# Kernel tuning notes

Hardware: AMD Instinct MI355X
Metric: run time of the kernel (lower is better)

Reference implementation:

```python
import jax, jax.numpy as jnp
import numpy as np

B, S, D = 8, 2048, 1024
N = 256          # state_dim
H = 512          # selector_hidden
E = 8            # num_experts


def murmurhash3_finalizer(token_ids):
    # Torch code works in int64 but masks to 32 bits after each multiply and
    # values stay non-negative, so it is exactly uint32 wrapping arithmetic.
    x = token_ids.astype(jnp.uint32)
    x = x ^ (x >> 16)
    x = x * jnp.uint32(2246822507)
    x = x ^ (x >> 13)
    x = x * jnp.uint32(3266489909)
    x = x ^ (x >> 16)
    return x


def setup_inputs() -> dict:
    key = jax.random.key(0)
    ks = jax.random.split(key, 7)
    scale = 0.02
    return {
        "x": jax.random.normal(ks[0], (B, S, D), dtype=jnp.float32),
        "token_ids": jax.random.randint(ks[1], (B, S), 0, 50257, dtype=jnp.int32),
        "Win": jax.random.normal(ks[2], (E, N, D), dtype=jnp.float32) * scale,      # in_proj.weight per expert
        "Wsin": jax.random.normal(ks[3], (E, H, D), dtype=jnp.float32) * scale,     # selector_in.weight
        "Wsout": jax.random.normal(ks[4], (E, 4 * N, H), dtype=jnp.float32) * scale,  # selector_out.weight
        "Wout": jax.random.normal(ks[5], (E, D, N), dtype=jnp.float32) * scale,     # out_proj.weight
        "dparam": jnp.ones((E, N), dtype=jnp.float32),                              # per-expert d
    }


def _forward(x, Win, Wsin, Wsout, Wout, dparam, token_ids):
    b, s, d = x.shape
    e_num, n, _ = Win.shape
    routes = (murmurhash3_finalizer(token_ids) % jnp.uint32(e_num)).astype(jnp.int32)  # (B,S)

    # Per-token expert projections, selected by hash route (masked accumulation
    # over the small fixed expert count; honors per-token routing).
    u = jnp.zeros((b, s, n), x.dtype)
    a = jnp.zeros((b, s, n), x.dtype)
    bg = jnp.zeros((b, s, n), x.dtype)
    c = jnp.zeros((b, s, n), x.dtype)
    dg = jnp.zeros((b, s, n), x.dtype)
    for e in range(e_num):
        m = (routes == e)[..., None]
        u = jnp.where(m, jnp.einsum('bsd,nd->bsn', x, Win[e]), u)
        sh = jax.nn.silu(jnp.einsum('bsd,hd->bsh', x, Wsin[e]))
        sel = jnp.einsum('bsh,oh->bso', sh, Wsout[e])       # (B,S,4N)
        ar, br, cr, dr = jnp.split(sel, 4, axis=-1)
        a = jnp.where(m, jax.nn.sigmoid(ar), a)
        bg = jnp.where(m, jnp.tanh(br), bg)
        c = jnp.where(m, jnp.tanh(cr), c)
        dg = jnp.where(m, jax.nn.sigmoid(dr), dg)

    dvec = dparam[routes]              # (B,S,N) expert d param per token
    skip = dvec * dg * u               # residual term, state-independent

    bidx = jnp.arange(b)

    def step(states, inp):
        # states: (B,E,N) per-expert hidden state per batch row
        route_t, u_t, a_t, b_t, c_t, skip_t = inp
        h_prev = states[bidx, route_t]                 # (B,N)
        h = a_t * h_prev + b_t * u_t
        states = states.at[bidx, route_t].set(h)       # only routed expert updates
        y = c_t * h + skip_t
        return states, y

    xs = (routes.swapaxes(0, 1), u.swapaxes(0, 1), a.swapaxes(0, 1),
          bg.swapaxes(0, 1), c.swapaxes(0, 1), skip.swapaxes(0, 1))
    states0 = jnp.zeros((b, e_num, n), x.dtype)
    _, ys = jax.lax.scan(step, states0, xs)            # ys: (S,B,N)
    y = ys.swapaxes(0, 1)                              # (B,S,N)

    out = jnp.zeros((b, s, d), x.dtype)
    for e in range(e_num):
        m = (routes == e)[..., None]
        out = jnp.where(m, jnp.einsum('bsn,dn->bsd', y, Wout[e]), out)
    return out


def reference(x, token_ids, Win, Wsin, Wsout, Wout, dparam):
    return _forward(x, Win, Wsin, Wsout, Wout, dparam, token_ids)
```

## Files before the change

### kernel.cpp

```cpp
#include <hip/hip_runtime.h>


#define TOKS 16384
#define RPAD 16512
#define DD   1024
#define NN   256
#define HH   512
#define MAXTILES  136
#define MAXCHUNKS 1088
#define CHUNK 16

typedef short short8 __attribute__((ext_vector_type(8)));
typedef float floatx4 __attribute__((ext_vector_type(4)));

#define AS_GLOBAL __attribute__((address_space(1)))
#define AS_LDS    __attribute__((address_space(3)))

__device__ __forceinline__ void gl_lds16(const void* g, void* l) {
    __builtin_amdgcn_global_load_lds((const AS_GLOBAL void*)g, (AS_LDS void*)l, 16, 0, 0);
}

__device__ __forceinline__ unsigned short f2bf(float f) {
    union { float f; unsigned u; } c; c.f = f;
    unsigned r = c.u + 0x7FFF + ((c.u >> 16) & 1);
    return (unsigned short)(r >> 16);
}
__device__ __forceinline__ int route_of(int token) {
    unsigned x = (unsigned)token;
    x ^= x >> 16; x *= 2246822507u; x ^= x >> 13; x *= 3266489909u; x ^= x >> 16;
    return (int)(x & 7u);
}
__device__ __forceinline__ float sigm(float v) { return 1.0f / (1.0f + __expf(-v)); }

__global__ void k_route(const int* __restrict__ tok, int* __restrict__ cnt) {
    int b = blockIdx.x, tid = threadIdx.x;
    __shared__ int lc[256 * 8];
    #pragma unroll
    for (int e = 0; e < 8; e++) lc[tid * 8 + e] = 0;
    #pragma unroll
    for (int i = 0; i < 8; i++) {
        int e = route_of(tok[b * 2048 + tid * 8 + i]);
        lc[tid * 8 + e]++;
    }
    __syncthreads();
    if (tid < 8) {
        int s = 0;
        for (int t = 0; t < 256; t++) s += lc[t * 8 + tid];
        cnt[b * 8 + tid] = s;
    }
}

__global__ void k_offsets(const int* __restrict__ cnt, int* __restrict__ grpoff,
                          int* __restrict__ tileE, int* __restrict__ tileS,
                          int* __restrict__ tileR,
                          int* __restrict__ cGrp, int* __restrict__ cStart,
                          int* __restrict__ cLen, int* __restrict__ gBase,
                          int* __restrict__ meta) {
    __shared__ int sc[64], ce[8], eoff[9], etile[9], gb[65], go[64];
    int tid = threadIdx.x;
    if (tid < 64) sc[tid] = cnt[tid];
    __syncthreads();
    if (tid < 8) { int s = 0; for (int b = 0; b < 8; b++) s += sc[b * 8 + tid]; ce[tid] = s; }
    __syncthreads();
    if (tid == 0) {
        eoff[0] = 0; etile[0] = 0;
        for (int e = 0; e < 8; e++) {
            eoff[e + 1] = eoff[e] + ce[e];
            etile[e + 1] = etile[e] + (ce[e] + 127) / 128;
        }
        meta[0] = etile[8];
        gb[0] = 0;
        for (int g = 0; g < 64; g++) gb[g + 1] = gb[g] + (sc[g] + CHUNK - 1) / CHUNK;
        meta[1] = gb[64];
    }
    __syncthreads();
    if (tid < 64) {
        int b = tid >> 3, e = tid & 7;
        int run = eoff[e];
        for (int b2 = 0; b2 < b; b2++) run += sc[b2 * 8 + e];
        go[tid] = run;
        grpoff[tid] = run;
    }
    __syncthreads();
    if (tid < 8) {
        int e = tid, st = eoff[e], c = ce[e], t0 = etile[e];
        for (int i = 0, k = 0; i < c; i += 128, k++) {
            tileE[t0 + k] = e; tileS[t0 + k] = st + i;
            tileR[t0 + k] = (c - i < 128) ? (c - i) : 128;
        }
    }
    if (tid < 64) {
        int g = tid, n = sc[g], base = gb[g], s0 = go[g];
        gBase[g] = base;
        for (int i = 0, c = 0; i < n; i += CHUNK, c++) {
            cGrp[base + c] = g;
            cStart[base + c] = s0 + i;
            cLen[base + c] = (n - i < CHUNK) ? (n - i) : CHUNK;
        }
    }
}

__global__ void k_scatter(const int* __restrict__ tok, const int* __restrict__ grpoff,
                          int* __restrict__ perm) {
    int b = blockIdx.x, tid = threadIdx.x;
    __shared__ int lh[8 * 256];
    int r[8];
    int myc[8] = {0,0,0,0,0,0,0,0};
    #pragma unroll
    for (int i = 0; i < 8; i++) {
        int e = route_of(tok[b * 2048 + tid * 8 + i]);
        r[i] = e; myc[e]++;
    }
    #pragma unroll
    for (int e = 0; e < 8; e++) lh[e * 256 + tid] = myc[e];
    __syncthreads();
    for (int e = 0; e < 8; e++) {
        for (int off = 1; off < 256; off <<= 1) {
            int add = (tid >= off) ? lh[e * 256 + tid - off] : 0;
            __syncthreads();
            lh[e * 256 + tid] += add;
            __syncthreads();
        }
    }
    int basep[8];
    #pragma unroll
    for (int e = 0; e < 8; e++) basep[e] = grpoff[b * 8 + e] + lh[e * 256 + tid] - myc[e];
    #pragma unroll
    for (int i = 0; i < 8; i++) {
        int e = r[i];
        perm[basep[e]++] = b * 2048 + tid * 8 + i;
    }
}

__global__ void k_cvtw(const float* __restrict__ Win, const float* __restrict__ Wsin,
                       const float* __restrict__ Wsout, const float* __restrict__ Wout,
                       unsigned short* __restrict__ W12, unsigned short* __restrict__ Wso,
                       unsigned short* __restrict__ Wo) {
    const int C12 = 8 * 768 * 1024 / 4, CSO = 8 * 1024 * 512 / 4, CWO = 8 * 1024 * 256 / 4;
    int c = blockIdx.x * 256 + threadIdx.x;
    float4 v; unsigned short* dst;
    if (c < C12) {
        int d = c * 4;
        int e = d / (768 * 1024);
        int rem = d - e * (768 * 1024);
        int r = rem >> 10, k = rem & 1023;
        const float* src = (r < 256) ? (Win + (((size_t)e * 256 + r) << 10) + k)
                                     : (Wsin + (((size_t)e * 512 + (r - 256)) << 10) + k);
        v = *(const float4*)src;
        dst = W12 + d;
    } else if (c < C12 + CSO) {
        int d = (c - C12) * 4;
        v = *(const float4*)(Wsout + d);
        dst = Wso + d;
    } else if (c < C12 + CSO + CWO) {
        int d = (c - C12 - CSO) * 4;
        v = *(const float4*)(Wout + d);
        dst = Wo + d;
    } else return;
    ushort4 o;
    o.x = f2bf(v.x); o.y = f2bf(v.y); o.z = f2bf(v.z); o.w = f2bf(v.w);
    *(ushort4*)dst = o;
}

__global__ void k_gather(const float* __restrict__ x, const int* __restrict__ perm,
                         unsigned short* __restrict__ Xs, unsigned short* __restrict__ SHb,
                         unsigned short* __restrict__ Yb) {
    int r = blockIdx.x, t = threadIdx.x;
    if (r < TOKS) {
        int tok = perm[r];
        float4 v = *(const float4*)(x + (size_t)tok * 1024 + t * 4);
        ushort4 o;
        o.x = f2bf(v.x); o.y = f2bf(v.y); o.z = f2bf(v.z); o.w = f2bf(v.w);
        *(ushort4*)(Xs + (size_t)r * 1024 + t * 4) = o;
    } else {
        ushort4 z = {0, 0, 0, 0};
        *(ushort4*)(Xs + (size_t)r * 1024 + t * 4) = z;
        if (t < 128) *(ushort4*)(SHb + (size_t)r * 512 + t * 4) = z;
        if (t < 64)  *(ushort4*)(Yb + (size_t)r * 256 + t * 4) = z;
    }
}

template<int MODE, int KD>
__global__ __launch_bounds__(256)
void k_mfma(const unsigned short* __restrict__ A, const unsigned short* __restrict__ Bw,
            const int* __restrict__ perm, const float* __restrict__ dparam,
            float* __restrict__ U, unsigned short* __restrict__ SHb,
            float* __restrict__ Aa, float* __restrict__ Wg,
            float* __restrict__ Cc, float* __restrict__ Sk,
            float* __restrict__ out,
            const int* __restrict__ tileE, const int* __restrict__ tileS,
            const int* __restrict__ tileR, const int* __restrict__ meta) {
    int mt = blockIdx.x;
    if (mt >= meta[0]) return;
    const int e = tileE[mt], pos0 = tileS[mt], rows = tileR[mt];
    const int col0 = blockIdx.y * 128;
    const int tid = threadIdx.x;
    const int w = tid >> 6, lane = tid & 63, quad = lane >> 4, l15 = lane & 15;
    const int wm = w & 1, wn = w >> 1;
    constexpr int NOUT = (MODE == 0) ? 768 : 1024;

    __shared__ unsigned short As[128 * 32];
    __shared__ unsigned short Bs[128 * 32];

    const int r0 = tid >> 2, c8 = (tid & 3) * 8;
    const unsigned short* ga = A + (size_t)(pos0 + r0) * KD + c8;
    const unsigned short* gb = Bw + ((size_t)e * NOUT + col0 + r0) * KD + c8;

    floatx4 acc[4][4] = {};

    int aoff[4], boff[4];
    #pragma unroll
    for (int i = 0; i < 4; i++) aoff[i] = (wm * 64 + i * 16 + l15) * 32 + quad * 8;
    #pragma unroll
    for (int j = 0; j < 4; j++) boff[j] = (wn * 64 + j * 16 + l15) * 32 + quad * 8;

    for (int k0 = 0; k0 < KD; k0 += 32) {
        __syncthreads();
        gl_lds16(ga + k0,                      As + w * 512);
        gl_lds16(ga + (size_t)64 * KD + k0,    As + 2048 + w * 512);
        gl_lds16(gb + k0,                      Bs + w * 512);
        gl_lds16(gb + (size_t)64 * KD + k0,    Bs + 2048 + w * 512);
        __syncthreads();
        short8 af[4], bf[4];
        #pragma unroll
        for (int i = 0; i < 4; i++) af[i] = *(const short8*)(As + aoff[i]);
        #pragma unroll
        for (int j = 0; j < 4; j++) bf[j] = *(const short8*)(Bs + boff[j]);
        #pragma unroll
        for (int i = 0; i < 4; i++)
            #pragma unroll
            for (int j = 0; j < 4; j++)
                acc[i][j] = __builtin_amdgcn_mfma_f32_16x16x32_bf16(af[i], bf[j], acc[i][j], 0, 0, 0);
    }

    #pragma unroll
    for (int i = 0; i < 4; i++) {
        #pragma unroll
        for (int r = 0; r < 4; r++) {
            int m = wm * 64 + i * 16 + quad * 4 + r;
            if (m >= rows) continue;
            size_t row = (size_t)(pos0 + m);
            if (MODE == 0) {
                if (col0 < 256) {
                    #pragma unroll
                    for (int j = 0; j < 4; j++) {
                        int n = col0 + wn * 64 + j * 16 + l15;
                        U[row * 256 + n] = acc[i][j][r];
                    }
                } else {
                    #pragma unroll
                    for (int j = 0; j < 4; j++) {
                        int n = col0 - 256 + wn * 64 + j * 16 + l15;
                        float v = acc[i][j][r];
                        SHb[row * 512 + n] = f2bf(v * sigm(v));
                    }
                }
            } else if (MODE == 1) {
                int region = col0 >> 8;
                #pragma unroll
                for (int j = 0; j < 4; j++) {
                    int n0 = (col0 & 255) + wn * 64 + j * 16 + l15;
                    size_t idx = row * 256 + (size_t)(n0 & 255);
                    float v = acc[i][j][r];
                    if (region == 0) {
                        Aa[idx] = sigm(v);
                    } else if (region == 1) {
                        Wg[idx] = tanhf(v) * U[idx];
                    } else if (region == 2) {
                        Cc[idx] = tanhf(v);
                    } else {
                        Sk[idx] = dparam[e * 256 + (n0 & 255)] * sigm(v) * U[idx];
                    }
                }
            } else {
                int tok = perm[row];
                #pragma unroll
                for (int j = 0; j < 4; j++) {
                    int n = col0 + wn * 64 + j * 16 + l15;
                    out[(size_t)tok * 1024 + n] = acc[i][j][r];
                }
            }
        }
    }
}

__global__ void k_scanA(const float* __restrict__ Aa, const float* __restrict__ Wg,
                        const int* __restrict__ cStart, const int* __restrict__ cLen,
                        const int* __restrict__ meta,
                        float* __restrict__ SA, float* __restrict__ SQ) {
    int id = blockIdx.x;
    if (id >= meta[1]) return;
    int t = threadIdx.x;
    int s0 = cStart[id], L = cLen[id];
    size_t idx = (size_t)s0 * 256 + t;
    float p = 1.0f, q = 0.0f;
    for (int i = 0; i < L; i++) {
        float a = Aa[idx], ww = Wg[idx];
        q = a * q + ww;
        p *= a;
        idx += 256;
    }
    SA[(size_t)id * 256 + t] = p;
    SQ[(size_t)id * 256 + t] = q;
}

__global__ void k_scanB(const float* __restrict__ SA, const float* __restrict__ SQ,
                        const int* __restrict__ gBase, const int* __restrict__ cnt,
                        float* __restrict__ Hin) {
    int g = blockIdx.x, t = threadIdx.x;
    int base = gBase[g], nch = (cnt[g] + CHUNK - 1) / CHUNK;
    float h = 0.0f;
    for (int c = 0; c < nch; c++) {
        size_t k = (size_t)(base + c) * 256 + t;
        Hin[k] = h;
        h = SA[k] * h + SQ[k];
    }
}

__global__ void k_scanC(const float* __restrict__ Aa, const float* __restrict__ Wg,
                        const float* __restrict__ Cc, const float* __restrict__ Sk,
                        const int* __restrict__ cStart, const int* __restrict__ cLen,
                        const int* __restrict__ meta, const float* __restrict__ Hin,
                        unsigned short* __restrict__ Yb) {
    int id = blockIdx.x;
    if (id >= meta[1]) return;
    int t = threadIdx.x;
    int s0 = cStart[id], L = cLen[id];
    float h = Hin[(size_t)id * 256 + t];
    size_t idx = (size_t)s0 * 256 + t;
    for (int i = 0; i < L; i++) {
        float a = Aa[idx], ww = Wg[idx], c = Cc[idx], sk = Sk[idx];
        h = a * h + ww;
        Yb[idx] = f2bf(c * h + sk);
        idx += 256;
    }
}

extern "C" void kernel_launch(void* const* d_in, const int* in_sizes, int n_in,
                              void* d_out, int out_size, void* d_ws, size_t ws_size,
                              hipStream_t stream) {
    const float* xin   = (const float*)d_in[0];
    const int*   tok   = (const int*)d_in[1];
    const float* Win   = (const float*)d_in[2];
    const float* Wsin  = (const float*)d_in[3];
    const float* Wsout = (const float*)d_in[4];
    const float* Wout  = (const float*)d_in[5];
    const float* dpar  = (const float*)d_in[6];
    float* out = (float*)d_out;

    size_t off = 0;
    char* base = (char*)d_ws;
    auto alloc = [&](size_t bytes) -> void* {
        void* p = base + off;
        off += (bytes + 255) & ~(size_t)255;
        return p;
    };
    float*          U   = (float*)alloc((size_t)RPAD * NN * 4);
    unsigned short* SHb = (unsigned short*)alloc((size_t)RPAD * HH * 2);
    unsigned short* Xs  = (unsigned short*)alloc((size_t)RPAD * DD * 2);
    unsigned short* Yb  = (unsigned short*)alloc((size_t)RPAD * NN * 2);
    float* Aa = (float*)alloc((size_t)TOKS * NN * 4);
    float* Wg = (float*)alloc((size_t)TOKS * NN * 4);
    float* Cc = (float*)alloc((size_t)TOKS * NN * 4);
    float* Sk = (float*)alloc((size_t)TOKS * NN * 4);
    unsigned short* W12 = (unsigned short*)alloc((size_t)8 * 768 * 1024 * 2);
    unsigned short* Wso = (unsigned short*)alloc((size_t)8 * 1024 * 512 * 2);
    unsigned short* Wo  = (unsigned short*)alloc((size_t)8 * 1024 * 256 * 2);
    float* SA  = (float*)alloc((size_t)MAXCHUNKS * 256 * 4);
    float* SQ  = (float*)alloc((size_t)MAXCHUNKS * 256 * 4);
    float* Hin = (float*)alloc((size_t)MAXCHUNKS * 256 * 4);
    int* perm   = (int*)alloc(TOKS * 4);
    int* cnt    = (int*)alloc(64 * 4);
    int* grpoff = (int*)alloc(64 * 4);
    int* tileE  = (int*)alloc(MAXTILES * 4);
    int* tileS  = (int*)alloc(MAXTILES * 4);
    int* tileR  = (int*)alloc(MAXTILES * 4);
    int* cGrp   = (int*)alloc(MAXCHUNKS * 4);
    int* cStart = (int*)alloc(MAXCHUNKS * 4);
    int* cLen   = (int*)alloc(MAXCHUNKS * 4);
    int* gBase  = (int*)alloc(64 * 4);
    int* meta   = (int*)alloc(16 * 4);

    k_route<<<8, 256, 0, stream>>>(tok, cnt);
    k_offsets<<<1, 256, 0, stream>>>(cnt, grpoff, tileE, tileS, tileR,
                                     cGrp, cStart, cLen, gBase, meta);
    k_scatter<<<8, 256, 0, stream>>>(tok, grpoff, perm);
    k_cvtw<<<12288, 256, 0, stream>>>(Win, Wsin, Wsout, Wout, W12, Wso, Wo);
    k_gather<<<RPAD, 256, 0, stream>>>(xin, perm, Xs, SHb, Yb);

    k_mfma<0, 1024><<<dim3(MAXTILES, 6), 256, 0, stream>>>(Xs, W12, perm, dpar,
        U, SHb, Aa, Wg, Cc, Sk, out, tileE, tileS, tileR, meta);
    k_mfma<1, 512><<<dim3(MAXTILES, 8), 256, 0, stream>>>(SHb, Wso, perm, dpar,
        U, SHb, Aa, Wg, Cc, Sk, out, tileE, tileS, tileR, meta);

    k_scanA<<<MAXCHUNKS, 256, 0, stream>>>(Aa, Wg, cStart, cLen, meta, SA, SQ);
    k_scanB<<<64, 256, 0, stream>>>(SA, SQ, gBase, cnt, Hin);
    k_scanC<<<MAXCHUNKS, 256, 0, stream>>>(Aa, Wg, Cc, Sk, cStart, cLen, meta, Hin, Yb);

    k_mfma<2, 256><<<dim3(MAXTILES, 8), 256, 0, stream>>>(Yb, Wo, perm, dpar,
        U, SHb, Aa, Wg, Cc, Sk, out, tileE, tileS, tileR, meta);
}
```

Measured before the change: 369.9 us.

## Store scan intermediates in fp16, double K-step in MFMA, fast tanh

Intermediate gate tensors (U, a, b*u, c, skip) are now stored as fp16 instead of fp32, halving their memory traffic in the GEMM epilogues and the scan kernels. The MFMA loop loads a 64-wide K slab per barrier pair instead of 32, halving the synchronisation count, and launch bounds request 3 waves per SIMD. tanhf is replaced by an exp-based formula. In exchange, fp16 storage and the approximate tanh reduce accuracy, and the doubled LDS footprint may limit occupancy.

```diff
diff --git a/kernel.cpp b/kernel.cpp
--- a/kernel.cpp
+++ b/kernel.cpp
@@ -12,6 +12,7 @@
 
 typedef short short8 __attribute__((ext_vector_type(8)));
 typedef float floatx4 __attribute__((ext_vector_type(4)));
+typedef _Float16 half_t;
 
 #define AS_GLOBAL __attribute__((address_space(1)))
 #define AS_LDS    __attribute__((address_space(3)))
@@ -31,6 +32,10 @@
     return (int)(x & 7u);
 }
 __device__ __forceinline__ float sigm(float v) { return 1.0f / (1.0f + __expf(-v)); }
+__device__ __forceinline__ float ftanh(float v) {
+    float e = __expf(2.0f * v);
+    return 1.0f - 2.0f / (e + 1.0f);
+}
 
 __global__ void k_route(const int* __restrict__ tok, int* __restrict__ cnt) {
     int b = blockIdx.x, tid = threadIdx.x;
@@ -181,12 +186,12 @@
 }
 
 template<int MODE, int KD>
-__global__ __launch_bounds__(256)
+__global__ __launch_bounds__(256, 3)
 void k_mfma(const unsigned short* __restrict__ A, const unsigned short* __restrict__ Bw,
             const int* __restrict__ perm, const float* __restrict__ dparam,
-            float* __restrict__ U, unsigned short* __restrict__ SHb,
-            float* __restrict__ Aa, float* __restrict__ Wg,
-            float* __restrict__ Cc, float* __restrict__ Sk,
+            half_t* __restrict__ Ub, unsigned short* __restrict__ SHb,
+            half_t* __restrict__ Aa, half_t* __restrict__ Wg,
+            half_t* __restrict__ Cc, half_t* __restrict__ Sk,
             float* __restrict__ out,
             const int* __restrict__ tileE, const int* __restrict__ tileS,
             const int* __restrict__ tileR, const int* __restrict__ meta) {
@@ -199,8 +204,8 @@
     const int wm = w & 1, wn = w >> 1;
     constexpr int NOUT = (MODE == 0) ? 768 : 1024;
 
-    __shared__ unsigned short As[128 * 32];
-    __shared__ unsigned short Bs[128 * 32];
+    __shared__ unsigned short As[2 * 128 * 32];
+    __shared__ unsigned short Bs[2 * 128 * 32];
 
     const int r0 = tid >> 2, c8 = (tid & 3) * 8;
     const unsigned short* ga = A + (size_t)(pos0 + r0) * KD + c8;
@@ -214,23 +219,30 @@
     #pragma unroll
     for (int j = 0; j < 4; j++) boff[j] = (wn * 64 + j * 16 + l15) * 32 + quad * 8;
 
-    for (int k0 = 0; k0 < KD; k0 += 32) {
+    for (int k0 = 0; k0 < KD; k0 += 64) {
         __syncthreads();
-        gl_lds16(ga + k0,                      As + w * 512);
-        gl_lds16(ga + (size_t)64 * KD + k0,    As + 2048 + w * 512);
-        gl_lds16(gb + k0,                      Bs + w * 512);
-        gl_lds16(gb + (size_t)64 * KD + k0,    Bs + 2048 + w * 512);
+        gl_lds16(ga + k0,                          As + w * 512);
+        gl_lds16(ga + (size_t)64 * KD + k0,        As + 2048 + w * 512);
+        gl_lds16(ga + k0 + 32,                     As + 4096 + w * 512);
+        gl_lds16(ga + (size_t)64 * KD + k0 + 32,   As + 6144 + w * 512);
+        gl_lds16(gb + k0,                          Bs + w * 512);
+        gl_lds16(gb + (size_t)64 * KD + k0,        Bs + 2048 + w * 512);
+        gl_lds16(gb + k0 + 32,                     Bs + 4096 + w * 512);
+        gl_lds16(gb + (size_t)64 * KD + k0 + 32,   Bs + 6144 + w * 512);
         __syncthreads();
-        short8 af[4], bf[4];
         #pragma unroll
-        for (int i = 0; i < 4; i++) af[i] = *(const short8*)(As + aoff[i]);
-        #pragma unroll
-        for (int j = 0; j < 4; j++) bf[j] = *(const short8*)(Bs + boff[j]);
-        #pragma unroll
-        for (int i = 0; i < 4; i++)
+        for (int kb = 0; kb < 2; kb++) {
+            short8 af[4], bf[4];
             #pragma unroll
-            for (int j = 0; j < 4; j++)
-                acc[i][j] = __builtin_amdgcn_mfma_f32_16x16x32_bf16(af[i], bf[j], acc[i][j], 0, 0, 0);
+            for (int i = 0; i < 4; i++) af[i] = *(const short8*)(As + kb * 4096 + aoff[i]);
+            #pragma unroll
+            for (int j = 0; j < 4; j++) bf[j] = *(const short8*)(Bs + kb * 4096 + boff[j]);
+            #pragma unroll
+            for (int i = 0; i < 4; i++)
+                #pragma unroll
+                for (int j = 0; j < 4; j++)
+                    acc[i][j] = __builtin_amdgcn_mfma_f32_16x16x32_bf16(af[i], bf[j], acc[i][j], 0, 0, 0);
+        }
     }
 
     #pragma unroll
@@ -245,7 +257,7 @@
                     #pragma unroll
                     for (int j = 0; j < 4; j++) {
                         int n = col0 + wn * 64 + j * 16 + l15;
-                        U[row * 256 + n] = acc[i][j][r];
+                        Ub[row * 256 + n] = (half_t)acc[i][j][r];
                     }
                 } else {
                     #pragma unroll
@@ -260,16 +272,16 @@
                 #pragma unroll
                 for (int j = 0; j < 4; j++) {
                     int n0 = (col0 & 255) + wn * 64 + j * 16 + l15;
-                    size_t idx = row * 256 + (size_t)(n0 & 255);
+                    size_t idx = row * 256 + (size_t)n0;
                     float v = acc[i][j][r];
                     if (region == 0) {
-                        Aa[idx] = sigm(v);
+                        Aa[idx] = (half_t)sigm(v);
                     } else if (region == 1) {
-                        Wg[idx] = tanhf(v) * U[idx];
+                        Wg[idx] = (half_t)(ftanh(v) * (float)Ub[idx]);
                     } else if (region == 2) {
-                        Cc[idx] = tanhf(v);
+                        Cc[idx] = (half_t)ftanh(v);
                     } else {
-                        Sk[idx] = dparam[e * 256 + (n0 & 255)] * sigm(v) * U[idx];
+                        Sk[idx] = (half_t)(dparam[e * 256 + n0] * sigm(v) * (float)Ub[idx]);
                     }
                 }
             } else {
@@ -284,7 +296,7 @@
     }
 }
 
-__global__ void k_scanA(const float* __restrict__ Aa, const float* __restrict__ Wg,
+__global__ void k_scanA(const half_t* __restrict__ Aa, const half_t* __restrict__ Wg,
                         const int* __restrict__ cStart, const int* __restrict__ cLen,
                         const int* __restrict__ meta,
                         float* __restrict__ SA, float* __restrict__ SQ) {
@@ -295,7 +307,7 @@
     size_t idx = (size_t)s0 * 256 + t;
     float p = 1.0f, q = 0.0f;
     for (int i = 0; i < L; i++) {
-        float a = Aa[idx], ww = Wg[idx];
+        float a = (float)Aa[idx], ww = (float)Wg[idx];
         q = a * q + ww;
         p *= a;
         idx += 256;
@@ -317,8 +329,8 @@
     }
 }
 
-__global__ void k_scanC(const float* __restrict__ Aa, const float* __restrict__ Wg,
-                        const float* __restrict__ Cc, const float* __restrict__ Sk,
+__global__ void k_scanC(const half_t* __restrict__ Aa, const half_t* __restrict__ Wg,
+                        const half_t* __restrict__ Cc, const half_t* __restrict__ Sk,
                         const int* __restrict__ cStart, const int* __restrict__ cLen,
                         const int* __restrict__ meta, const float* __restrict__ Hin,
                         unsigned short* __restrict__ Yb) {
@@ -329,7 +341,8 @@
     float h = Hin[(size_t)id * 256 + t];
     size_t idx = (size_t)s0 * 256 + t;
     for (int i = 0; i < L; i++) {
-        float a = Aa[idx], ww = Wg[idx], c = Cc[idx], sk = Sk[idx];
+        float a = (float)Aa[idx], ww = (float)Wg[idx];
+        float c = (float)Cc[idx], sk = (float)Sk[idx];
         h = a * h + ww;
         Yb[idx] = f2bf(c * h + sk);
         idx += 256;
@@ -355,14 +368,14 @@
         off += (bytes + 255) & ~(size_t)255;
         return p;
     };
-    float*          U   = (float*)alloc((size_t)RPAD * NN * 4);
+    half_t*         Ub  = (half_t*)alloc((size_t)RPAD * NN * 2);
     unsigned short* SHb = (unsigned short*)alloc((size_t)RPAD * HH * 2);
     unsigned short* Xs  = (unsigned short*)alloc((size_t)RPAD * DD * 2);
     unsigned short* Yb  = (unsigned short*)alloc((size_t)RPAD * NN * 2);
-    float* Aa = (float*)alloc((size_t)TOKS * NN * 4);
-    float* Wg = (float*)alloc((size_t)TOKS * NN * 4);
-    float* Cc = (float*)alloc((size_t)TOKS * NN * 4);
-    float* Sk = (float*)alloc((size_t)TOKS * NN * 4);
+    half_t* Aa = (half_t*)alloc((size_t)TOKS * NN * 2);
+    half_t* Wg = (half_t*)alloc((size_t)TOKS * NN * 2);
+    half_t* Cc = (half_t*)alloc((size_t)TOKS * NN * 2);
+    half_t* Sk = (half_t*)alloc((size_t)TOKS * NN * 2);
     unsigned short* W12 = (unsigned short*)alloc((size_t)8 * 768 * 1024 * 2);
     unsigned short* Wso = (unsigned short*)alloc((size_t)8 * 1024 * 512 * 2);
     unsigned short* Wo  = (unsigned short*)alloc((size_t)8 * 1024 * 256 * 2);
@@ -389,14 +402,14 @@
     k_gather<<<RPAD, 256, 0, stream>>>(xin, perm, Xs, SHb, Yb);
 
     k_mfma<0, 1024><<<dim3(MAXTILES, 6), 256, 0, stream>>>(Xs, W12, perm, dpar,
-        U, SHb, Aa, Wg, Cc, Sk, out, tileE, tileS, tileR, meta);
+        Ub, SHb, Aa, Wg, Cc, Sk, out, tileE, tileS, tileR, meta);
     k_mfma<1, 512><<<dim3(MAXTILES, 8), 256, 0, stream>>>(SHb, Wso, perm, dpar,
-        U, SHb, Aa, Wg, Cc, Sk, out, tileE, tileS, tileR, meta);
+        Ub, SHb, Aa, Wg, Cc, Sk, out, tileE, tileS, tileR, meta);
 
     k_scanA<<<MAXCHUNKS, 256, 0, stream>>>(Aa, Wg, cStart, cLen, meta, SA, SQ);
     k_scanB<<<64, 256, 0, stream>>>(SA, SQ, gBase, cnt, Hin);
     k_scanC<<<MAXCHUNKS, 256, 0, stream>>>(Aa, Wg, Cc, Sk, cStart, cLen, meta, Hin, Yb);
 
     k_mfma<2, 256><<<dim3(MAXTILES, 8), 256, 0, stream>>>(Yb, Wo, perm, dpar,
-        U, SHb, Aa, Wg, Cc, Sk, out, tileE, tileS, tileR, meta);
-}
+        Ub, SHb, Aa, Wg, Cc, Sk, out, tileE, tileS, tileR, meta);
+}
```

Result: faster. 322.9 us (-12.7%).
